# Optimization experiments

Measured on AMD Instinct MI355X. Metric: run time of the kernel, lower is better.

## Reference

```python
import jax, jax.numpy as jnp
import numpy as np

V = 50257
D = 512
T = 1024


def setup_inputs() -> dict:
    key = jax.random.key(0)
    ks = jax.random.split(key, 12)
    si = (2.0 / (V + D)) ** 0.5   # xavier-ish scale for input matrices
    sh = (1.0 / D) ** 0.5         # scale for recurrent matrices
    so = (2.0 / (V + D)) ** 0.5
    return {
        "idx": jax.random.randint(ks[0], (T,), 0, V, dtype=jnp.int32),
        "W_ii": jax.random.normal(ks[1], (D, V), jnp.float32) * si,
        "W_if": jax.random.normal(ks[2], (D, V), jnp.float32) * si,
        "W_io": jax.random.normal(ks[3], (D, V), jnp.float32) * si,
        "W_ig": jax.random.normal(ks[4], (D, V), jnp.float32) * si,
        "W_hi": jax.random.normal(ks[5], (D, D), jnp.float32) * sh,
        "W_hf": jax.random.normal(ks[6], (D, D), jnp.float32) * sh,
        "W_ho": jax.random.normal(ks[7], (D, D), jnp.float32) * sh,
        "W_hg": jax.random.normal(ks[8], (D, D), jnp.float32) * sh,
        "b_i": jnp.zeros((D,), jnp.float32),
        "b_f": jnp.ones((D,), jnp.float32),
        "b_o": jnp.zeros((D,), jnp.float32),
        "b_g": jnp.zeros((D,), jnp.float32),
        "W_out": jax.random.normal(ks[9], (V, D), jnp.float32) * so,
        "b_out": jnp.zeros((V,), jnp.float32),
    }


def reference(idx, W_ii, W_if, W_io, W_ig, W_hi, W_hf, W_ho, W_hg,
              b_i, b_f, b_o, b_g, W_out, b_out):
    # One-hot @ W.T == column gather: W[:, tok]. Dropout is identity (eval mode).
    dims = W_hi.shape[0]

    def step(carry, tok):
        h, c = carry
        i = jax.nn.sigmoid(W_ii[:, tok] + b_i + W_hi @ h)
        f = jax.nn.sigmoid(W_if[:, tok] + b_f + W_hf @ h)
        o = jax.nn.sigmoid(W_io[:, tok] + b_o + W_ho @ h)
        g = jnp.tanh(W_ig[:, tok] + b_g + W_hg @ h)
        c_new = f * c + i * g
        h_new = o * jnp.tanh(c_new)
        logits = W_out @ h_new + b_out          # [V]
        return (h_new, c_new), jax.nn.log_softmax(logits)

    h0 = jnp.zeros((dims,), W_hi.dtype)
    c0 = jnp.zeros((dims,), W_hi.dtype)
    (h, c), log_probs = jax.lax.scan(step, (h0, c0), idx)
    return log_probs, h, c  # log_probs: [T, V]
```

## Files before the change

### kernel.cpp

```cpp
#include <hip/hip_runtime.h>
#include <hip/hip_bf16.h>

#define VV 50257
#define DD 512
#define TT 1024
#define VPADN 50304
#define NBR 64
#define WCB 128

typedef __bf16 bf16;
typedef __attribute__((ext_vector_type(8))) __bf16 bf16x8;
typedef __attribute__((ext_vector_type(4))) __bf16 bf16x4;
typedef __attribute__((ext_vector_type(4))) float f32x4;
typedef __attribute__((ext_vector_type(4))) unsigned int u32x4;

__device__ __forceinline__ void gload_lds16(const void* g, void* l) {
  __builtin_amdgcn_global_load_lds(
      (__attribute__((address_space(1))) void*)(void*)g,
      (__attribute__((address_space(3))) void*)l, 16, 0, 0);
}

__global__ __launch_bounds__(512) void recur_fused_kernel(
    const int* __restrict__ idx,
    const float* __restrict__ Wii, const float* __restrict__ Wif,
    const float* __restrict__ Wio, const float* __restrict__ Wig,
    const float* __restrict__ Whi, const float* __restrict__ Whf,
    const float* __restrict__ Who, const float* __restrict__ Whg,
    const float* __restrict__ bi, const float* __restrict__ bfv,
    const float* __restrict__ bo, const float* __restrict__ bg,
    const float* __restrict__ Wout,
    unsigned long long* __restrict__ Hpack, bf16* __restrict__ Hbf,
    bf16* __restrict__ Wbf, float* __restrict__ out_tail) {
  __shared__ f32x4 wlds[8][4][2][64];
  __shared__ f32x4 hsh[2][128];
  const int b = blockIdx.x, tid = threadIdx.x;

  if (b >= NBR) {
    const int wb = b - NBR;
    const size_t nch = (size_t)VPADN * DD / 4;
    for (size_t i = (size_t)wb * 512 + tid; i < nch; i += (size_t)WCB * 512) {
      size_t e = i << 2;
      bf16x4 o;
      if ((e >> 9) < VV) {
        f32x4 x = *(const f32x4*)&Wout[e];
        o[0] = (bf16)x[0]; o[1] = (bf16)x[1]; o[2] = (bf16)x[2]; o[3] = (bf16)x[3];
      } else {
        o[0] = o[1] = o[2] = o[3] = (bf16)0.f;
      }
      *(bf16x4*)&Wbf[e] = o;
    }
    return;
  }

  const int lane = tid & 63, w = tid >> 6;
  const int hd = (b << 3) + w;

  {
    #pragma unroll
    for (int g = 0; g < 4; ++g) {
      const float* Wg = (g == 0) ? Whi : (g == 1) ? Whf : (g == 2) ? Who : Whg;
      #pragma unroll
      for (int j = 0; j < 2; ++j)
        wlds[w][g][j][lane] = *(const f32x4*)&Wg[(size_t)hd*DD + (j << 8) + (lane << 2)];
    }
  }

  const float* wxp = nullptr;
  float bias = 0.f;
  if (lane < 4) {
    const float* Wx = (lane == 0) ? Wii : (lane == 1) ? Wif : (lane == 2) ? Wio : Wig;
    const float* bx = (lane == 0) ? bi : (lane == 1) ? bfv : (lane == 2) ? bo : bg;
    wxp = &Wx[(size_t)hd * VV];
    bias = bx[hd];
  }
  float c = 0.f;
  __syncthreads();

  for (int t = 0; t < TT; ++t) {
    const int tok = idx[t];
    float xv = 0.f;
    if (lane < 4) xv = wxp[tok] + bias;

    f32x4* hb = hsh[t & 1];
    if (t > 0) {
      if (tid < 256) {
        const unsigned long long* src = &Hpack[(size_t)(t-1)*DD + (tid << 1)];
        u32x4 v;
        for (;;) {
          asm volatile("global_load_dwordx4 %0, %1, off sc1\n\t"
                       "s_waitcnt vmcnt(0)"
                       : "=v"(v) : "v"(src) : "memory");
          if (v[1] == (unsigned)t && v[3] == (unsigned)t) break;
          __builtin_amdgcn_s_sleep(1);
        }
        ((float2*)hb)[tid] = float2{__uint_as_float(v[0]), __uint_as_float(v[2])};
      }
    } else {
      if (tid < 256) ((float2*)hb)[tid] = float2{0.f, 0.f};
    }
    __syncthreads();

    const f32x4 h0 = hb[lane], h1 = hb[64 + lane];
    f32x4 m0 = wlds[w][0][0][lane]*h0 + wlds[w][0][1][lane]*h1;
    f32x4 m1 = wlds[w][1][0][lane]*h0 + wlds[w][1][1][lane]*h1;
    f32x4 m2 = wlds[w][2][0][lane]*h0 + wlds[w][2][1][lane]*h1;
    f32x4 m3 = wlds[w][3][0][lane]*h0 + wlds[w][3][1][lane]*h1;
    float a0 = m0[0]+m0[1]+m0[2]+m0[3];
    float a1 = m1[0]+m1[1]+m1[2]+m1[3];
    float a2 = m2[0]+m2[1]+m2[2]+m2[3];
    float a3 = m3[0]+m3[1]+m3[2]+m3[3];
    #pragma unroll
    for (int mask = 1; mask < 64; mask <<= 1) {
      a0 += __shfl_xor(a0, mask);
      a1 += __shfl_xor(a1, mask);
      a2 += __shfl_xor(a2, mask);
      a3 += __shfl_xor(a3, mask);
    }

    float myacc = (lane == 0) ? a0 : (lane == 1) ? a1 : (lane == 2) ? a2 : a3;
    float pre = myacc + xv;
    bool isg = (lane == 3);
    float e1 = __expf(isg ? -2.f * pre : -pre);
    float rr = 1.f / (1.f + e1);
    float act = isg ? (2.f * rr - 1.f) : rr;

    float ia = __shfl(act, 0);
    float fa = __shfl(act, 1);
    float oa = __shfl(act, 2);
    float ga = __shfl(act, 3);

    if (lane == 0) {
      c = fa * c + ia * ga;
      float e2 = __expf(-2.f * c);
      float th = 2.f / (1.f + e2) - 1.f;
      float h = oa * th;
      unsigned long long pk =
          ((unsigned long long)(unsigned)(t + 1) << 32) | (unsigned long long)__float_as_uint(h);
      __hip_atomic_store(&Hpack[(size_t)t*DD + hd], pk, __ATOMIC_RELAXED,
                         __HIP_MEMORY_SCOPE_AGENT);
      Hbf[(size_t)t*DD + hd] = (bf16)h;
      if (t == TT - 1) { out_tail[hd] = h; out_tail[DD + hd] = c; }
    }
  }
}

__global__ __launch_bounds__(256, 2) void gemm_kernel(
    const bf16* __restrict__ A, const bf16* __restrict__ B,
    const float* __restrict__ bout, float* __restrict__ Cout) {
  __shared__ bf16 As[128*32];
  __shared__ bf16 Bs[128*32];
  const int tid = threadIdx.x;
  const int n0 = blockIdx.x * 128, m0 = blockIdx.y * 128;
  const int w = tid >> 6, l = tid & 63;
  const int wr = w >> 1, wc = w & 1;
  f32x4 acc[4][4] = {};

  for (int k0 = 0; k0 < DD; k0 += 32) {
    #pragma unroll
    for (int c = 0; c < 2; ++c) {
      int j = c*256 + tid;
      int row = j >> 2, kc = (j & 3) << 3;
      gload_lds16(&A[(size_t)(m0 + row)*DD + k0 + kc], (char*)As + (c*4096 + w*1024));
      gload_lds16(&B[(size_t)(n0 + row)*DD + k0 + kc], (char*)Bs + (c*4096 + w*1024));
    }
    __syncthreads();
    bf16x8 af[4], bfr[4];
    #pragma unroll
    for (int mi = 0; mi < 4; ++mi)
      af[mi] = *(const bf16x8*)&As[(wr*64 + mi*16 + (l & 15))*32 + (l >> 4)*8];
    #pragma unroll
    for (int ni = 0; ni < 4; ++ni)
      bfr[ni] = *(const bf16x8*)&Bs[(wc*64 + ni*16 + (l & 15))*32 + (l >> 4)*8];
    #pragma unroll
    for (int mi = 0; mi < 4; ++mi)
      #pragma unroll
      for (int ni = 0; ni < 4; ++ni)
        acc[mi][ni] = __builtin_amdgcn_mfma_f32_16x16x32_bf16(af[mi], bfr[ni], acc[mi][ni], 0, 0, 0);
    __syncthreads();
  }

  #pragma unroll
  for (int mi = 0; mi < 4; ++mi) {
    int rbase = m0 + wr*64 + mi*16 + (l >> 4)*4;
    #pragma unroll
    for (int ni = 0; ni < 4; ++ni) {
      int col = n0 + wc*64 + ni*16 + (l & 15);
      if (col < VV) {
        float bb = bout[col];
        #pragma unroll
        for (int r = 0; r < 4; ++r)
          Cout[(size_t)(rbase + r)*VV + col] = acc[mi][ni][r] + bb;
      }
    }
  }
}

__global__ __launch_bounds__(256) void lsm_kernel(float* __restrict__ logits) {
  const int t = blockIdx.x, tid = threadIdx.x;
  float* row = logits + (size_t)t*VV;
  float m = -INFINITY, s = 0.f;
  for (int v = tid; v < VV; v += 256) {
    float x = row[v];
    float nm = fmaxf(m, x);
    s = s*expf(m - nm) + expf(x - nm);
    m = nm;
  }
  #pragma unroll
  for (int mask = 1; mask < 64; mask <<= 1) {
    float om = __shfl_xor(m, mask);
    float os = __shfl_xor(s, mask);
    float nm = fmaxf(m, om);
    s = s*expf(m - nm) + os*expf(om - nm);
    m = nm;
  }
  __shared__ float sm[4], ss[4], lse_sh;
  int wv = tid >> 6;
  if ((tid & 63) == 0) { sm[wv] = m; ss[wv] = s; }
  __syncthreads();
  if (tid == 0) {
    float M = sm[0], S = ss[0];
    for (int i2 = 1; i2 < 4; ++i2) {
      float nm = fmaxf(M, sm[i2]);
      S = S*expf(M - nm) + ss[i2]*expf(sm[i2] - nm);
      M = nm;
    }
    lse_sh = M + logf(S);
  }
  __syncthreads();
  float lse = lse_sh;
  for (int v = tid; v < VV; v += 256)
    row[v] -= lse;
}

extern "C" void kernel_launch(void* const* d_in, const int* in_sizes, int n_in,
                              void* d_out, int out_size, void* d_ws, size_t ws_size,
                              hipStream_t stream) {
  const int*   idx  = (const int*)d_in[0];
  const float* Wii  = (const float*)d_in[1];
  const float* Wif  = (const float*)d_in[2];
  const float* Wio  = (const float*)d_in[3];
  const float* Wig  = (const float*)d_in[4];
  const float* Whi  = (const float*)d_in[5];
  const float* Whf  = (const float*)d_in[6];
  const float* Who  = (const float*)d_in[7];
  const float* Whg  = (const float*)d_in[8];
  const float* bi   = (const float*)d_in[9];
  const float* bfv  = (const float*)d_in[10];
  const float* bo   = (const float*)d_in[11];
  const float* bg   = (const float*)d_in[12];
  const float* Wout = (const float*)d_in[13];
  const float* bout = (const float*)d_in[14];
  float* out = (float*)d_out;

  char* ws = (char*)d_ws;
  bf16*  Wbf  = (bf16*)ws;
  unsigned long long* Hpack = (unsigned long long*)(ws + 51511296);
  bf16*  Hbf  = (bf16*)(ws + 55705600);

  hipMemsetAsync(Hpack, 0, (size_t)TT*DD*8, stream);
  recur_fused_kernel<<<NBR + WCB, 512, 0, stream>>>(
      idx, Wii, Wif, Wio, Wig, Whi, Whf, Who, Whg, bi, bfv, bo, bg, Wout,
      Hpack, Hbf, Wbf, out + (size_t)TT*VV);
  gemm_kernel<<<dim3(393, 8), 256, 0, stream>>>(Hbf, Wbf, bout, out);
  lsm_kernel<<<TT, 256, 0, stream>>>(out);
}
```

Measured before the change: 2.283 ms.

## Keep recurrent weights in registers and poll h with all threads

Moves each wave's recurrent-weight slices out of LDS into VGPRs, pinned there with empty asm barriers, and caches the token indices in LDS. Every one of the 512 threads now polls one 8-byte packed h element, with no sleep, instead of 256 threads polling 16-byte pairs with a sleep. It also sets waves_per_eu(2,2) to give the compiler a register budget. This is meant to cut LDS traffic and latency on the serial per-step critical path, at the cost of more polling traffic on global memory.

```diff
diff --git a/kernel.cpp b/kernel.cpp
--- a/kernel.cpp
+++ b/kernel.cpp
@@ -12,7 +12,6 @@
 typedef __attribute__((ext_vector_type(8))) __bf16 bf16x8;
 typedef __attribute__((ext_vector_type(4))) __bf16 bf16x4;
 typedef __attribute__((ext_vector_type(4))) float f32x4;
-typedef __attribute__((ext_vector_type(4))) unsigned int u32x4;
 
 __device__ __forceinline__ void gload_lds16(const void* g, void* l) {
   __builtin_amdgcn_global_load_lds(
@@ -20,7 +19,8 @@
       (__attribute__((address_space(3))) void*)l, 16, 0, 0);
 }
 
-__global__ __launch_bounds__(512) void recur_fused_kernel(
+__global__ __launch_bounds__(512) __attribute__((amdgpu_waves_per_eu(2, 2)))
+void recur_fused_kernel(
     const int* __restrict__ idx,
     const float* __restrict__ Wii, const float* __restrict__ Wif,
     const float* __restrict__ Wio, const float* __restrict__ Wig,
@@ -31,8 +31,8 @@
     const float* __restrict__ Wout,
     unsigned long long* __restrict__ Hpack, bf16* __restrict__ Hbf,
     bf16* __restrict__ Wbf, float* __restrict__ out_tail) {
-  __shared__ f32x4 wlds[8][4][2][64];
-  __shared__ f32x4 hsh[2][128];
+  __shared__ float hsh[2][DD];
+  __shared__ int idxs[TT];
   const int b = blockIdx.x, tid = threadIdx.x;
 
   if (b >= NBR) {
@@ -52,17 +52,25 @@
     return;
   }
 
+  idxs[tid] = idx[tid];
+  idxs[tid + 512] = idx[tid + 512];
+
   const int lane = tid & 63, w = tid >> 6;
   const int hd = (b << 3) + w;
 
+  f32x4 wr0[4], wr1[4];
   {
     #pragma unroll
     for (int g = 0; g < 4; ++g) {
       const float* Wg = (g == 0) ? Whi : (g == 1) ? Whf : (g == 2) ? Who : Whg;
-      #pragma unroll
-      for (int j = 0; j < 2; ++j)
-        wlds[w][g][j][lane] = *(const f32x4*)&Wg[(size_t)hd*DD + (j << 8) + (lane << 2)];
-    }
+      wr0[g] = *(const f32x4*)&Wg[(size_t)hd*DD + (lane << 2)];
+      wr1[g] = *(const f32x4*)&Wg[(size_t)hd*DD + 256 + (lane << 2)];
+    }
+  }
+  #pragma unroll
+  for (int g = 0; g < 4; ++g) {
+    asm volatile("" : "+v"(wr0[g]));
+    asm volatile("" : "+v"(wr1[g]));
   }
 
   const float* wxp = nullptr;
@@ -77,34 +85,30 @@
   __syncthreads();
 
   for (int t = 0; t < TT; ++t) {
-    const int tok = idx[t];
     float xv = 0.f;
-    if (lane < 4) xv = wxp[tok] + bias;
-
-    f32x4* hb = hsh[t & 1];
+    if (lane < 4) xv = wxp[idxs[t]] + bias;
+
+    float* hb = hsh[t & 1];
     if (t > 0) {
-      if (tid < 256) {
-        const unsigned long long* src = &Hpack[(size_t)(t-1)*DD + (tid << 1)];
-        u32x4 v;
-        for (;;) {
-          asm volatile("global_load_dwordx4 %0, %1, off sc1\n\t"
-                       "s_waitcnt vmcnt(0)"
-                       : "=v"(v) : "v"(src) : "memory");
-          if (v[1] == (unsigned)t && v[3] == (unsigned)t) break;
-          __builtin_amdgcn_s_sleep(1);
-        }
-        ((float2*)hb)[tid] = float2{__uint_as_float(v[0]), __uint_as_float(v[2])};
-      }
+      const unsigned long long* src = &Hpack[(size_t)(t-1)*DD + tid];
+      unsigned long long v;
+      do {
+        asm volatile("global_load_dwordx2 %0, %1, off sc1\n\t"
+                     "s_waitcnt vmcnt(0)"
+                     : "=v"(v) : "v"(src) : "memory");
+      } while (__builtin_expect((unsigned)(v >> 32) != (unsigned)t, 0));
+      hb[tid] = __uint_as_float((unsigned)v);
     } else {
-      if (tid < 256) ((float2*)hb)[tid] = float2{0.f, 0.f};
+      hb[tid] = 0.f;
     }
     __syncthreads();
 
-    const f32x4 h0 = hb[lane], h1 = hb[64 + lane];
-    f32x4 m0 = wlds[w][0][0][lane]*h0 + wlds[w][0][1][lane]*h1;
-    f32x4 m1 = wlds[w][1][0][lane]*h0 + wlds[w][1][1][lane]*h1;
-    f32x4 m2 = wlds[w][2][0][lane]*h0 + wlds[w][2][1][lane]*h1;
-    f32x4 m3 = wlds[w][3][0][lane]*h0 + wlds[w][3][1][lane]*h1;
+    const f32x4 h0 = *(const f32x4*)&hb[lane << 2];
+    const f32x4 h1 = *(const f32x4*)&hb[256 + (lane << 2)];
+    f32x4 m0 = wr0[0]*h0 + wr1[0]*h1;
+    f32x4 m1 = wr0[1]*h0 + wr1[1]*h1;
+    f32x4 m2 = wr0[2]*h0 + wr1[2]*h1;
+    f32x4 m3 = wr0[3]*h0 + wr1[3]*h1;
     float a0 = m0[0]+m0[1]+m0[2]+m0[3];
     float a1 = m1[0]+m1[1]+m1[2]+m1[3];
     float a2 = m2[0]+m2[1]+m2[2]+m2[3];
```

Result: faster. 2.061 ms (-9.7%).
